# Kernel optimization log

Hardware: AMD Instinct MI355X
Metric: run time of the kernel (lower is better)

## Reference

```python
import jax, jax.numpy as jnp
import numpy as np

D_MODEL = 1024
N_HEAD = 16
POWER = 4
EPS = 1e-6
MASK_FILL = -1000.0


def setup_inputs() -> dict:
    key = jax.random.key(0)
    ks = jax.random.split(key, 10)
    B, T, C = 2, 2048, D_MODEL
    sc = 1.0 / np.sqrt(C)
    inp = {
        "x": jax.random.normal(ks[0], (B, T, C), jnp.float32),
        "Wq": jax.random.normal(ks[1], (C, C), jnp.float32) * sc,
        "bq": jnp.zeros((C,), jnp.float32),
        "Wk": jax.random.normal(ks[2], (C, C), jnp.float32) * sc,
        "bk": jnp.zeros((C,), jnp.float32),
        "Wv": jax.random.normal(ks[3], (C, C), jnp.float32) * sc,
        "bv": jnp.zeros((C,), jnp.float32),
        "Wo": jax.random.normal(ks[4], (C, C), jnp.float32) * sc,
        "bo": jnp.zeros((C,), jnp.float32),
        "score_gain": jnp.asarray(4.0, jnp.float32),
        # True above the diagonal -> masked (causal)
        "causal_mask": jnp.triu(jnp.ones((T, T), jnp.bool_), k=1),
    }
    return inp


def rational_softmax(x):
    s = x / (jnp.abs(x) + 1.0)          # squash to (-1, 1)
    p = ((s + 1.0) * 0.5) ** POWER      # (0,1) then sharpen
    return p / (jnp.sum(p, axis=-1, keepdims=True) + EPS)


def reference(x, Wq, bq, Wk, bk, Wv, bv, Wo, bo, score_gain, causal_mask):
    B, T, C = x.shape
    H, D = N_HEAD, C // N_HEAD
    q = (x @ Wq + bq).reshape(B, T, H, D)
    k = (x @ Wk + bk).reshape(B, T, H, D)
    v = (x @ Wv + bv).reshape(B, T, H, D)
    # scores: (B, H, T, T)
    scores = jnp.einsum('bqhd,bkhd->bhqk', q, k)
    scores = scores - jnp.mean(scores, axis=-1, keepdims=True)
    mad = jnp.mean(jnp.abs(scores), axis=-1, keepdims=True) + 1e-6
    scores = scores / mad * score_gain
    scores = jnp.where(causal_mask, MASK_FILL, scores)
    attn = rational_softmax(scores)
    out = jnp.einsum('bhqk,bkhd->bqhd', attn, v).reshape(B, T, C)
    return out @ Wo + bo
```

## Files before the change

### kernel.cpp

```cpp
#include <hip/hip_runtime.h>
#include <hip/hip_bf16.h>
#include <cstdint>

#define BDIM 2
#define TSEQ 2048
#define CDIM 1024
#define NH 16
#define HD 64
#define NTOK (BDIM*TSEQ)
#define MASK_FILL_V (-1000.0f)
#define EPS_V (1e-6f)

typedef short bf16x8 __attribute__((ext_vector_type(8)));
typedef float f32x4  __attribute__((ext_vector_type(4)));

__device__ __forceinline__ float bf2f(unsigned short u) {
    union { unsigned int i; float f; } x; x.i = ((unsigned int)u) << 16; return x.f;
}
__device__ __forceinline__ unsigned short f2bf(float v) {
    __hip_bfloat16 h = __float2bfloat16(v);
    union { __hip_bfloat16 h; unsigned short u; } c; c.h = h; return c.u;
}
__device__ __forceinline__ float unpk_lo(unsigned int u) {
    union { unsigned int i; float f; } x; x.i = u << 16; return x.f;
}
__device__ __forceinline__ float unpk_hi(unsigned int u) {
    union { unsigned int i; float f; } x; x.i = u & 0xFFFF0000u; return x.f;
}
__device__ __forceinline__ unsigned int pk2(float lo, float hi) {
    unsigned int r;
    asm("v_cvt_pk_bf16_f32 %0, %1, %2" : "=v"(r) : "v"(lo), "v"(hi));
    return r;
}

__device__ __forceinline__ bool dt_is_bf16(const void* gain_p) {
    return ((*(const unsigned int*)gain_p) & 0xFFFFu) == 0x4080u;
}
__device__ __forceinline__ float ld1(const void* p, size_t i, bool bf) {
    return bf ? bf2f(((const unsigned short*)p)[i]) : ((const float*)p)[i];
}

__device__ __forceinline__ void gl2lds16(const unsigned short* g, unsigned short* l) {
    __builtin_amdgcn_global_load_lds(
        (const __attribute__((address_space(1))) unsigned int*)g,
        (__attribute__((address_space(3))) unsigned int*)l, 16, 0, 0);
}

__global__ __launch_bounds__(256) void pack_x_kernel(
    const void* __restrict__ X, const void* __restrict__ gain_p,
    unsigned short* __restrict__ Xb)
{
    const bool bf = dt_is_bf16(gain_p);
    size_t i = ((size_t)blockIdx.x * 256 + threadIdx.x) * 8;
    if (bf) {
        *(bf16x8*)&Xb[i] = *(const bf16x8*)((const unsigned short*)X + i);
    } else {
        const float* xf = (const float*)X;
        float4 a = *(const float4*)&xf[i];
        float4 b = *(const float4*)&xf[i + 4];
        bf16x8 o;
        o[0]=(short)f2bf(a.x); o[1]=(short)f2bf(a.y); o[2]=(short)f2bf(a.z); o[3]=(short)f2bf(a.w);
        o[4]=(short)f2bf(b.x); o[5]=(short)f2bf(b.y); o[6]=(short)f2bf(b.z); o[7]=(short)f2bf(b.w);
        *(bf16x8*)&Xb[i] = o;
    }
}

__global__ __launch_bounds__(256) void pack_wt_kernel(
    const void* __restrict__ Wq, const void* __restrict__ Wk,
    const void* __restrict__ Wv, const void* __restrict__ Wo,
    const void* __restrict__ gain_p, unsigned short* __restrict__ Wt)
{
    __shared__ __align__(16) unsigned short tile[64][72];
    const bool bf = dt_is_bf16(gain_p);
    const int which = blockIdx.z;
    const void* W = (which == 0) ? Wq : (which == 1) ? Wk : (which == 2) ? Wv : Wo;
    const int k0 = blockIdx.y * 64, n0 = blockIdx.x * 64;
    const int t = threadIdx.x;
    const int r = t >> 2, cb = (t & 3) * 16;
    if (bf) {
        const unsigned short* wsd = (const unsigned short*)W;
        *(bf16x8*)&tile[r][cb]     = *(const bf16x8*)&wsd[(size_t)(k0 + r) * CDIM + n0 + cb];
        *(bf16x8*)&tile[r][cb + 8] = *(const bf16x8*)&wsd[(size_t)(k0 + r) * CDIM + n0 + cb + 8];
    } else {
        const float* wf = (const float*)W;
        const float* src = &wf[(size_t)(k0 + r) * CDIM + n0 + cb];
        float4 f0 = *(const float4*)&src[0];
        float4 f1 = *(const float4*)&src[4];
        float4 f2 = *(const float4*)&src[8];
        float4 f3 = *(const float4*)&src[12];
        bf16x8 o0, o1;
        o0[0]=(short)f2bf(f0.x); o0[1]=(short)f2bf(f0.y); o0[2]=(short)f2bf(f0.z); o0[3]=(short)f2bf(f0.w);
        o0[4]=(short)f2bf(f1.x); o0[5]=(short)f2bf(f1.y); o0[6]=(short)f2bf(f1.z); o0[7]=(short)f2bf(f1.w);
        o1[0]=(short)f2bf(f2.x); o1[1]=(short)f2bf(f2.y); o1[2]=(short)f2bf(f2.z); o1[3]=(short)f2bf(f2.w);
        o1[4]=(short)f2bf(f3.x); o1[5]=(short)f2bf(f3.y); o1[6]=(short)f2bf(f3.z); o1[7]=(short)f2bf(f3.w);
        *(bf16x8*)&tile[r][cb]     = o0;
        *(bf16x8*)&tile[r][cb + 8] = o1;
    }
    __syncthreads();
    const int dr = t >> 2, tb = (t & 3) * 16;
    __align__(16) unsigned short tmp[16];
#pragma unroll
    for (int j = 0; j < 16; ++j) tmp[j] = tile[tb + j][dr];
    unsigned short* dst = Wt + ((size_t)(which * CDIM + n0 + dr)) * CDIM + k0 + tb;
    *(bf16x8*)&dst[0] = *(bf16x8*)&tmp[0];
    *(bf16x8*)&dst[8] = *(bf16x8*)&tmp[8];
}

__global__ __launch_bounds__(256) void gemm_mfma_kernel(
    const unsigned short* __restrict__ A,
    const unsigned short* __restrict__ Bt,
    const void* __restrict__ b0p, const void* __restrict__ b1p,
    const void* __restrict__ b2p,
    const void* __restrict__ gain_p,
    unsigned short* __restrict__ qkv,
    void* __restrict__ outp, int mode)
{
    __shared__ __align__(16) unsigned short As[128 * 32];
    __shared__ __align__(16) unsigned short Bs[128 * 32];

    const bool bf = dt_is_bf16(gain_p);
    const int t = threadIdx.x;
    const int w = t >> 6, lane = t & 63, quad = lane >> 4, l16 = lane & 15;
    const int wm = w >> 1, wn = w & 1;
    const int n0 = blockIdx.x * 128, m0 = blockIdx.y * 128;

    const unsigned short* Ag = A  + (size_t)m0 * CDIM;
    const unsigned short* Bg = Bt + (size_t)n0 * CDIM;

    f32x4 acc[4][4];
#pragma unroll
    for (int mt = 0; mt < 4; ++mt)
#pragma unroll
        for (int nt = 0; nt < 4; ++nt)
            acc[mt][nt] = (f32x4){0.f, 0.f, 0.f, 0.f};

    for (int kt = 0; kt < CDIM / 32; ++kt) {
        const int k0 = kt * 32;
#pragma unroll
        for (int i = 0; i < 2; ++i) {
            const int chunk = (i * 4 + w) * 64 + lane;
            const int row = chunk >> 2, kp = (chunk & 3) * 8;
            gl2lds16(Ag + (size_t)row * CDIM + k0 + kp, &As[(i * 4 + w) * 512]);
            gl2lds16(Bg + (size_t)row * CDIM + k0 + kp, &Bs[(i * 4 + w) * 512]);
        }
        __syncthreads();
        bf16x8 af[4], bfr[4];
#pragma unroll
        for (int mt = 0; mt < 4; ++mt)
            af[mt] = *(const bf16x8*)&As[(wm * 64 + mt * 16 + l16) * 32 + quad * 8];
#pragma unroll
        for (int nt = 0; nt < 4; ++nt)
            bfr[nt] = *(const bf16x8*)&Bs[(wn * 64 + nt * 16 + l16) * 32 + quad * 8];
#pragma unroll
        for (int mt = 0; mt < 4; ++mt)
#pragma unroll
            for (int nt = 0; nt < 4; ++nt)
                acc[mt][nt] = __builtin_amdgcn_mfma_f32_16x16x32_bf16(af[mt], bfr[nt], acc[mt][nt], 0, 0, 0);
        __syncthreads();
    }

    if (mode == 0) {
        const int which = n0 >> 10;
        if (which < 2) {
            const void* biasP = (which == 0) ? b0p : b1p;
            unsigned short* out = qkv + (size_t)which * NTOK * CDIM;
#pragma unroll
            for (int nt = 0; nt < 4; ++nt) {
                const int np = (n0 & 1023) + wn * 64 + nt * 16 + l16;
                const int h = np >> 6, d = np & 63;
                const float bias = ld1(biasP, np, bf);
#pragma unroll
                for (int mt = 0; mt < 4; ++mt)
#pragma unroll
                    for (int r = 0; r < 4; ++r) {
                        const int m = m0 + wm * 64 + mt * 16 + quad * 4 + r;
                        const int bb = m >> 11, tt = m & (TSEQ - 1);
                        out[(((size_t)(bb * NH + h)) * TSEQ + tt) * HD + d] =
                            f2bf(acc[mt][nt][r] + bias);
                    }
            }
        } else {
            unsigned short* vt = (unsigned short*)outp;
#pragma unroll
            for (int nt = 0; nt < 4; ++nt) {
                const int np = (n0 & 1023) + wn * 64 + nt * 16 + l16;
                const int h = np >> 6, d = np & 63;
                const float bias = ld1(b2p, np, bf);
#pragma unroll
                for (int mt = 0; mt < 4; ++mt) {
                    const int m = m0 + wm * 64 + mt * 16 + quad * 4;
                    const int bb = m >> 11, tt0 = m & (TSEQ - 1);
                    unsigned int lo = ((unsigned int)f2bf(acc[mt][nt][1] + bias) << 16)
                                    |  (unsigned int)f2bf(acc[mt][nt][0] + bias);
                    unsigned int hi = ((unsigned int)f2bf(acc[mt][nt][3] + bias) << 16)
                                    |  (unsigned int)f2bf(acc[mt][nt][2] + bias);
                    uint2 pk; pk.x = lo; pk.y = hi;
                    *(uint2*)&vt[((size_t)(bb * NH + h) * HD + d) * TSEQ + tt0] = pk;
                }
            }
        }
    } else {
#pragma unroll
        for (int nt = 0; nt < 4; ++nt) {
            const int np = n0 + wn * 64 + nt * 16 + l16;
            const float bias = ld1(b0p, np, bf);
#pragma unroll
            for (int mt = 0; mt < 4; ++mt)
#pragma unroll
                for (int r = 0; r < 4; ++r) {
                    const int m = m0 + wm * 64 + mt * 16 + quad * 4 + r;
                    const float v = acc[mt][nt][r] + bias;
                    if (bf) ((__hip_bfloat16*)outp)[(size_t)m * CDIM + np] = __float2bfloat16(v);
                    else    ((float*)outp)[(size_t)m * CDIM + np] = v;
                }
        }
    }
}

__global__ __launch_bounds__(256) void ksum_kernel(
    const unsigned short* __restrict__ Kb, float* __restrict__ Ksum)
{
    __shared__ float red[32][64];
    const int bh = blockIdx.x;
    const int t = threadIdx.x;
    const int d8 = (t & 7) * 8, g = t >> 3;
    const unsigned short* kp = Kb + (size_t)bh * TSEQ * HD;
    float s[8] = {};
    for (int tt = g; tt < TSEQ; tt += 32) {
        bf16x8 v = *(const bf16x8*)&kp[(size_t)tt * HD + d8];
#pragma unroll
        for (int j = 0; j < 8; ++j) s[j] += bf2f((unsigned short)v[j]);
    }
#pragma unroll
    for (int j = 0; j < 8; ++j) red[g][d8 + j] = s[j];
    __syncthreads();
    if (t < 64) {
        float tot = 0.f;
#pragma unroll
        for (int gg = 0; gg < 32; ++gg) tot += red[gg][t];
        Ksum[(size_t)bh * HD + t] = tot;
    }
}

#define QROWS 16
#define NQT (TSEQ / QROWS)

__global__ __launch_bounds__(512, 2) void attn_mfma_kernel(
    const unsigned short* __restrict__ Qb,
    const unsigned short* __restrict__ Kb,
    const unsigned short* __restrict__ Vt,
    const float* __restrict__ Ksum,
    const void* __restrict__ gain_p,
    unsigned short* __restrict__ AOb)
{
    __shared__ float smad[2][8][16];
    __shared__ float spsum[2][8][16];
    __shared__ float pvp[8][16 * 68];

    const bool bf = dt_is_bf16(gain_p);
    const float gain = ld1(gain_p, 0, bf);

    const int t    = threadIdx.x;
    const int w    = t >> 6;
    const int lane = t & 63;
    const int quad = lane >> 4;
    const int l16  = lane & 15;
    const int b4   = quad & 1, b5 = quad >> 1;

    const int id = blockIdx.x;
    const int bh = id & 31;
    const int p  = id >> 5;
    const int q0a = p * QROWS;
    const int q0b = (NQT - 1 - p) * QROWS;
    const int b  = bh >> 4, h = bh & 15;
    const size_t base = (size_t)bh * TSEQ * HD;

    bf16x8 qfA[2], qfB[2];
    qfA[0] = *(const bf16x8*)&Qb[base + (size_t)(q0a + l16) * HD + quad * 8];
    qfA[1] = *(const bf16x8*)&Qb[base + (size_t)(q0a + l16) * HD + 32 + quad * 8];
    qfB[0] = *(const bf16x8*)&Qb[base + (size_t)(q0b + l16) * HD + quad * 8];
    qfB[1] = *(const bf16x8*)&Qb[base + (size_t)(q0b + l16) * HD + 32 + quad * 8];

    const float* Ks = Ksum + (size_t)bh * HD;
    float4 kA0 = *(const float4*)&Ks[quad * 8];
    float4 kA1 = *(const float4*)&Ks[quad * 8 + 4];
    float4 kB0 = *(const float4*)&Ks[32 + quad * 8];
    float4 kB1 = *(const float4*)&Ks[32 + quad * 8 + 4];
    auto qdot = [&](const bf16x8 (&qf)[2]) -> float {
        float m;
        m  = bf2f((unsigned short)qf[0][0]) * kA0.x;
        m  = fmaf(bf2f((unsigned short)qf[0][1]), kA0.y, m);
        m  = fmaf(bf2f((unsigned short)qf[0][2]), kA0.z, m);
        m  = fmaf(bf2f((unsigned short)qf[0][3]), kA0.w, m);
        m  = fmaf(bf2f((unsigned short)qf[0][4]), kA1.x, m);
        m  = fmaf(bf2f((unsigned short)qf[0][5]), kA1.y, m);
        m  = fmaf(bf2f((unsigned short)qf[0][6]), kA1.z, m);
        m  = fmaf(bf2f((unsigned short)qf[0][7]), kA1.w, m);
        m  = fmaf(bf2f((unsigned short)qf[1][0]), kB0.x, m);
        m  = fmaf(bf2f((unsigned short)qf[1][1]), kB0.y, m);
        m  = fmaf(bf2f((unsigned short)qf[1][2]), kB0.z, m);
        m  = fmaf(bf2f((unsigned short)qf[1][3]), kB0.w, m);
        m  = fmaf(bf2f((unsigned short)qf[1][4]), kB1.x, m);
        m  = fmaf(bf2f((unsigned short)qf[1][5]), kB1.y, m);
        m  = fmaf(bf2f((unsigned short)qf[1][6]), kB1.z, m);
        m  = fmaf(bf2f((unsigned short)qf[1][7]), kB1.w, m);
        m += __shfl_xor(m, 16);
        m += __shfl_xor(m, 32);
        return m * (1.0f / TSEQ);
    };
    const float meanA = qdot(qfA);
    const float meanB = qdot(qfB);

    const unsigned short* kp = Kb + base + (size_t)(w * 16 + l16) * HD + quad * 8;
    bf16x8 kbuf[4][2];
#pragma unroll
    for (int i = 0; i < 4; ++i) {
        kbuf[i][0] = *(const bf16x8*)&kp[(size_t)i * 8192];
        kbuf[i][1] = *(const bf16x8*)&kp[(size_t)i * 8192 + 32];
    }

    unsigned int pkwA[8][2], pkwB[16][2];
    float madpA0 = 0.f, madpA1 = 0.f, madpB0 = 0.f, madpB1 = 0.f;
#pragma unroll
    for (int i = 0; i < 16; ++i) {
        bf16x8 c0 = kbuf[i & 3][0], c1 = kbuf[i & 3][1];
        if (i + 4 < 16) {
            kbuf[i & 3][0] = *(const bf16x8*)&kp[(size_t)(i + 4) * 8192];
            kbuf[i & 3][1] = *(const bf16x8*)&kp[(size_t)(i + 4) * 8192 + 32];
        }
        f32x4 z = (f32x4){0.f, 0.f, 0.f, 0.f};
        f32x4 sA0 = __builtin_amdgcn_mfma_f32_16x16x32_bf16(c0, qfA[0], z, 0, 0, 0);
        f32x4 sA1 = __builtin_amdgcn_mfma_f32_16x16x32_bf16(c1, qfA[1], z, 0, 0, 0);
        f32x4 sB0 = __builtin_amdgcn_mfma_f32_16x16x32_bf16(c0, qfB[0], z, 0, 0, 0);
        f32x4 sB1 = __builtin_amdgcn_mfma_f32_16x16x32_bf16(c1, qfB[1], z, 0, 0, 0);
        float a0 = (sA0[0] + sA1[0]) - meanA, a1 = (sA0[1] + sA1[1]) - meanA;
        float a2 = (sA0[2] + sA1[2]) - meanA, a3 = (sA0[3] + sA1[3]) - meanA;
        madpA0 += fabsf(a0) + fabsf(a1);
        madpA1 += fabsf(a2) + fabsf(a3);
        if (i < 8) {
            pkwA[i][0] = pk2(a0, a1);
            pkwA[i][1] = pk2(a2, a3);
        }
        float e0 = (sB0[0] + sB1[0]) - meanB, e1 = (sB0[1] + sB1[1]) - meanB;
        float e2 = (sB0[2] + sB1[2]) - meanB, e3 = (sB0[3] + sB1[3]) - meanB;
        madpB0 += fabsf(e0) + fabsf(e1);
        madpB1 += fabsf(e2) + fabsf(e3);
        pkwB[i][0] = pk2(e0, e1);
        pkwB[i][1] = pk2(e2, e3);
    }
    float madpA = madpA0 + madpA1;
    float madpB = madpB0 + madpB1;
    madpA += __shfl_xor(madpA, 16);
    madpA += __shfl_xor(madpA, 32);
    madpB += __shfl_xor(madpB, 16);
    madpB += __shfl_xor(madpB, 32);
    if (lane < 16) { smad[0][w][lane] = madpA; smad[1][w][lane] = madpB; }
    __syncthreads();

    float msA = 0.f, msB = 0.f;
#pragma unroll
    for (int ww = 0; ww < 8; ++ww) { msA += smad[0][ww][l16]; msB += smad[1][ww][l16]; }
    const float scaleA = gain / (msA * (1.0f / TSEQ) + 1e-6f);
    const float scaleB = gain / (msB * (1.0f / TSEQ) + 1e-6f);

    const int NTmaxA = p;
    const int NTmaxB = NQT - 1 - p;
    const int difA = NTmaxA - w;
    const int i_maxA = (difA >= 0) ? (difA >> 3) : -1;
    const int jmaxA  = (i_maxA >= 0) ? (i_maxA >> 1) : -1;
    const int difB = NTmaxB - w;
    const int i_maxB = (difB >= 0) ? (difB >> 3) : -1;
    const int jmaxB  = (i_maxB >= 0) ? (i_maxB >> 1) : -1;

    const bool kgt0 = (quad * 4 + 0) > l16;
    const bool kgt1 = (quad * 4 + 1) > l16;
    const bool kgt2 = (quad * 4 + 2) > l16;
    const bool kgt3 = (quad * 4 + 3) > l16;

    auto rsoft = [](float vv) -> float {
        float rc = __builtin_amdgcn_rcpf(fabsf(vv) + 1.0f);
        float ss = vv * rc;
        float u  = fmaf(ss, 0.5f, 0.5f);
        float u2 = u * u;
        return u2 * u2;
    };
    auto xform = [&](unsigned int plo, unsigned int phi, bool mask, float scale,
                     float& psum, unsigned int& P0, unsigned int& P1) {
        float v0 = unpk_lo(plo) * scale, v1 = unpk_hi(plo) * scale;
        float v2 = unpk_lo(phi) * scale, v3 = unpk_hi(phi) * scale;
        if (mask) {
            if (kgt0) v0 = MASK_FILL_V;
            if (kgt1) v1 = MASK_FILL_V;
            if (kgt2) v2 = MASK_FILL_V;
            if (kgt3) v3 = MASK_FILL_V;
        }
        float p0 = rsoft(v0), p1 = rsoft(v1), p2 = rsoft(v2), p3 = rsoft(v3);
        psum += (p0 + p1) + (p2 + p3);
        P0 = pk2(p0, p1);
        P1 = pk2(p2, p3);
    };
    auto exch = [&](const unsigned int (&pk0)[2], const unsigned int (&pk1)[2],
                    bool use1, bool mask0, bool mask1, float scale,
                    float& psum, unsigned int (&fru)[4]) {
        unsigned int A0, A1, B0, B1;
        xform(pk0[0], pk0[1], mask0, scale, psum, A0, A1);
        if (use1) xform(pk1[0], pk1[1], mask1, scale, psum, B0, B1);
        else { B0 = 0u; B1 = 0u; }
        unsigned int K0 = b5 ? B0 : A0, K1 = b5 ? B1 : A1;
        unsigned int T0 = b5 ? A0 : B0, T1 = b5 ? A1 : B1;
        unsigned int R0 = (unsigned int)__shfl_xor((int)T0, 32);
        unsigned int R1 = (unsigned int)__shfl_xor((int)T1, 32);
        unsigned int S0 = (b5 ^ b4) ? K0 : R0, S1 = (b5 ^ b4) ? K1 : R1;
        unsigned int U0 = (unsigned int)__shfl_xor((int)S0, 16);
        unsigned int U1 = (unsigned int)__shfl_xor((int)S1, 16);
        fru[0] = b4 ? U0 : (b5 ? R0 : K0);
        fru[1] = b4 ? U1 : (b5 ? R1 : K1);
        fru[2] = b4 ? (b5 ? K0 : R0) : U0;
        fru[3] = b4 ? (b5 ? K1 : R1) : U1;
    };

    const unsigned short* vp = Vt + ((size_t)bh * HD + l16) * TSEQ
                               + w * 16 + b5 * 128 + b4 * 8;

    float psumA = 0.f, psumB = 0.f;
    f32x4 aA0 = (f32x4){0.f,0.f,0.f,0.f}, aA1 = (f32x4){0.f,0.f,0.f,0.f};
    f32x4 aA2 = (f32x4){0.f,0.f,0.f,0.f}, aA3 = (f32x4){0.f,0.f,0.f,0.f};
    f32x4 aB0 = (f32x4){0.f,0.f,0.f,0.f}, aB1 = (f32x4){0.f,0.f,0.f,0.f};
    f32x4 aB2 = (f32x4){0.f,0.f,0.f,0.f}, aB3 = (f32x4){0.f,0.f,0.f,0.f};
#pragma unroll
    for (int j = 0; j < 8; ++j) {
        if (j <= jmaxB) {
            bf16x8 vb0 = *(const bf16x8*)&vp[j * 256 + 0 * 32768];
            bf16x8 vb1 = *(const bf16x8*)&vp[j * 256 + 1 * 32768];
            bf16x8 vb2 = *(const bf16x8*)&vp[j * 256 + 2 * 32768];
            bf16x8 vb3 = *(const bf16x8*)&vp[j * 256 + 3 * 32768];
            unsigned int fruB[4];
            exch(pkwB[2 * j], pkwB[2 * j + 1], (2 * j + 1) <= i_maxB,
                 (w + 16 * j) == NTmaxB, (w + 16 * j + 8) == NTmaxB,
                 scaleB, psumB, fruB);
            union { unsigned int u[4]; bf16x8 v; } FB;
            FB.u[0] = fruB[0]; FB.u[1] = fruB[1]; FB.u[2] = fruB[2]; FB.u[3] = fruB[3];
            aB0 = __builtin_amdgcn_mfma_f32_16x16x32_bf16(FB.v, vb0, aB0, 0, 0, 0);
            aB1 = __builtin_amdgcn_mfma_f32_16x16x32_bf16(FB.v, vb1, aB1, 0, 0, 0);
            aB2 = __builtin_amdgcn_mfma_f32_16x16x32_bf16(FB.v, vb2, aB2, 0, 0, 0);
            aB3 = __builtin_amdgcn_mfma_f32_16x16x32_bf16(FB.v, vb3, aB3, 0, 0, 0);
            if (j < 4) {
                if (j <= jmaxA) {
                    unsigned int fruA[4];
                    exch(pkwA[2 * j], pkwA[2 * j + 1], (2 * j + 1) <= i_maxA,
                         (w + 16 * j) == NTmaxA, (w + 16 * j + 8) == NTmaxA,
                         scaleA, psumA, fruA);
                    union { unsigned int u[4]; bf16x8 v; } FA;
                    FA.u[0] = fruA[0]; FA.u[1] = fruA[1]; FA.u[2] = fruA[2]; FA.u[3] = fruA[3];
                    aA0 = __builtin_amdgcn_mfma_f32_16x16x32_bf16(FA.v, vb0, aA0, 0, 0, 0);
                    aA1 = __builtin_amdgcn_mfma_f32_16x16x32_bf16(FA.v, vb1, aA1, 0, 0, 0);
                    aA2 = __builtin_amdgcn_mfma_f32_16x16x32_bf16(FA.v, vb2, aA2, 0, 0, 0);
                    aA3 = __builtin_amdgcn_mfma_f32_16x16x32_bf16(FA.v, vb3, aA3, 0, 0, 0);
                }
            }
        }
    }

    psumA += __shfl_xor(psumA, 16);
    psumA += __shfl_xor(psumA, 32);
    psumB += __shfl_xor(psumB, 16);
    psumB += __shfl_xor(psumB, 32);
    if (lane < 16) { spsum[0][w][lane] = psumA; spsum[1][w][lane] = psumB; }

#pragma unroll
    for (int r = 0; r < 4; ++r) {
        const int qi = quad * 4 + r;
        pvp[w][qi * 68 +      l16] = aA0[r];
        pvp[w][qi * 68 + 16 + l16] = aA1[r];
        pvp[w][qi * 68 + 32 + l16] = aA2[r];
        pvp[w][qi * 68 + 48 + l16] = aA3[r];
    }
    __syncthreads();
    {
        const int q  = t >> 5;
        const int d2 = (t & 31) * 2;
        float s0 = 0.f, s1 = 0.f;
#pragma unroll
        for (int ww = 0; ww < 8; ++ww) {
            const float* pp = &pvp[ww][q * 68 + d2];
            s0 += pp[0];
            s1 += pp[1];
        }
        float ps = 0.f;
#pragma unroll
        for (int ww = 0; ww < 8; ++ww) ps += spsum[0][ww][q];
        const float inv = 1.0f / (ps + EPS_V);
        unsigned int o = ((unsigned int)f2bf(s1 * inv) << 16) | (unsigned int)f2bf(s0 * inv);
        *(unsigned int*)&AOb[((size_t)(b * TSEQ + q0a + q)) * CDIM + h * HD + d2] = o;
    }
    __syncthreads();

#pragma unroll
    for (int r = 0; r < 4; ++r) {
        const int qi = quad * 4 + r;
        pvp[w][qi * 68 +      l16] = aB0[r];
        pvp[w][qi * 68 + 16 + l16] = aB1[r];
        pvp[w][qi * 68 + 32 + l16] = aB2[r];
        pvp[w][qi * 68 + 48 + l16] = aB3[r];
    }
    __syncthreads();
    {
        const int q  = t >> 5;
        const int d2 = (t & 31) * 2;
        float s0 = 0.f, s1 = 0.f;
#pragma unroll
        for (int ww = 0; ww < 8; ++ww) {
            const float* pp = &pvp[ww][q * 68 + d2];
            s0 += pp[0];
            s1 += pp[1];
        }
        float ps = 0.f;
#pragma unroll
        for (int ww = 0; ww < 8; ++ww) ps += spsum[1][ww][q];
        const float inv = 1.0f / (ps + EPS_V);
        unsigned int o = ((unsigned int)f2bf(s1 * inv) << 16) | (unsigned int)f2bf(s0 * inv);
        *(unsigned int*)&AOb[((size_t)(b * TSEQ + q0b + q)) * CDIM + h * HD + d2] = o;
    }
}

extern "C" void kernel_launch(void* const* d_in, const int* in_sizes, int n_in,
                              void* d_out, int out_size, void* d_ws, size_t ws_size,
                              hipStream_t stream)
{
    (void)in_sizes; (void)n_in; (void)out_size; (void)ws_size;
    const void* X    = d_in[0];
    const void* Wq   = d_in[1];
    const void* bq   = d_in[2];
    const void* Wk   = d_in[3];
    const void* bk   = d_in[4];
    const void* Wv   = d_in[5];
    const void* bv   = d_in[6];
    const void* Wo   = d_in[7];
    const void* bo   = d_in[8];
    const void* gain = d_in[9];

    char* ws = (char*)d_ws;
    unsigned short* Xb  = (unsigned short*)ws;
    unsigned short* Wt  = (unsigned short*)(ws + (8ull  << 20));
    unsigned short* QKV = (unsigned short*)(ws + (16ull << 20));
    unsigned short* Vt  = (unsigned short*)(ws + (40ull << 20));
    unsigned short* AOb = (unsigned short*)(ws + (48ull << 20));
    float*          Ks  = (float*)(ws + (56ull << 20));
    unsigned short* Qb  = QKV;
    unsigned short* Kb  = QKV + (size_t)NTOK * CDIM;

    pack_x_kernel<<<NTOK * CDIM / (256 * 8), 256, 0, stream>>>(X, gain, Xb);
    pack_wt_kernel<<<dim3(16, 16, 4), 256, 0, stream>>>(Wq, Wk, Wv, Wo, gain, Wt);

    dim3 g1(3 * CDIM / 128, NTOK / 128);
    gemm_mfma_kernel<<<g1, 256, 0, stream>>>(Xb, Wt, bq, bk, bv, gain, QKV, Vt, 0);

    ksum_kernel<<<BDIM * NH, 256, 0, stream>>>(Kb, Ks);

    attn_mfma_kernel<<<(NQT / 2) * BDIM * NH, 512, 0, stream>>>(
        Qb, Kb, Vt, Ks, gain, AOb);

    dim3 g3(CDIM / 128, NTOK / 128);
    gemm_mfma_kernel<<<g3, 256, 0, stream>>>(AOb, Wt + 3ull * CDIM * CDIM, bo, bo, bo, gain,
                                             nullptr, d_out, 1);
}
```

Baseline: 309.7 us.

## Swizzle GEMM block order, fold mean into MFMA init, prefetch V, set MFMA priority

The GEMM remaps block indices so consecutive workgroups are spread across eight groups, aiming at better L2/XCD locality. In attention, the mean subtraction is folded into the MFMA accumulator init, which saves some VALU subtracts. The first V tile is now prefetched before the MAD reduction barrier so its load latency overlaps the sync. MFMA groups are also wrapped in s_setprio so the scheduler favours matrix issue. The swizzle assumes the grid size divides by eight.

```diff
diff --git a/kernel.cpp b/kernel.cpp
--- a/kernel.cpp
+++ b/kernel.cpp
@@ -122,7 +122,12 @@
     const int t = threadIdx.x;
     const int w = t >> 6, lane = t & 63, quad = lane >> 4, l16 = lane & 15;
     const int wm = w >> 1, wn = w & 1;
-    const int n0 = blockIdx.x * 128, m0 = blockIdx.y * 128;
+
+    const int gx = gridDim.x, gy = gridDim.y;
+    const int lin = blockIdx.y * gx + blockIdx.x;
+    const int chunk = (gx * gy) >> 3;
+    const int nid = (lin & 7) * chunk + (lin >> 3);
+    const int n0 = (nid / gy) * 128, m0 = (nid % gy) * 128;
 
     const unsigned short* Ag = A  + (size_t)m0 * CDIM;
     const unsigned short* Bg = Bt + (size_t)n0 * CDIM;
@@ -138,8 +143,8 @@
         const int k0 = kt * 32;
 #pragma unroll
         for (int i = 0; i < 2; ++i) {
-            const int chunk = (i * 4 + w) * 64 + lane;
-            const int row = chunk >> 2, kp = (chunk & 3) * 8;
+            const int chunkid = (i * 4 + w) * 64 + lane;
+            const int row = chunkid >> 2, kp = (chunkid & 3) * 8;
             gl2lds16(Ag + (size_t)row * CDIM + k0 + kp, &As[(i * 4 + w) * 512]);
             gl2lds16(Bg + (size_t)row * CDIM + k0 + kp, &Bs[(i * 4 + w) * 512]);
         }
@@ -310,6 +315,8 @@
     };
     const float meanA = qdot(qfA);
     const float meanB = qdot(qfB);
+    const f32x4 cinitA = (f32x4){-meanA, -meanA, -meanA, -meanA};
+    const f32x4 cinitB = (f32x4){-meanB, -meanB, -meanB, -meanB};
 
     const unsigned short* kp = Kb + base + (size_t)(w * 16 + l16) * HD + quad * 8;
     bf16x8 kbuf[4][2];
@@ -329,20 +336,20 @@
             kbuf[i & 3][1] = *(const bf16x8*)&kp[(size_t)(i + 4) * 8192 + 32];
         }
         f32x4 z = (f32x4){0.f, 0.f, 0.f, 0.f};
-        f32x4 sA0 = __builtin_amdgcn_mfma_f32_16x16x32_bf16(c0, qfA[0], z, 0, 0, 0);
+        f32x4 sA0 = __builtin_amdgcn_mfma_f32_16x16x32_bf16(c0, qfA[0], cinitA, 0, 0, 0);
         f32x4 sA1 = __builtin_amdgcn_mfma_f32_16x16x32_bf16(c1, qfA[1], z, 0, 0, 0);
-        f32x4 sB0 = __builtin_amdgcn_mfma_f32_16x16x32_bf16(c0, qfB[0], z, 0, 0, 0);
+        f32x4 sB0 = __builtin_amdgcn_mfma_f32_16x16x32_bf16(c0, qfB[0], cinitB, 0, 0, 0);
         f32x4 sB1 = __builtin_amdgcn_mfma_f32_16x16x32_bf16(c1, qfB[1], z, 0, 0, 0);
-        float a0 = (sA0[0] + sA1[0]) - meanA, a1 = (sA0[1] + sA1[1]) - meanA;
-        float a2 = (sA0[2] + sA1[2]) - meanA, a3 = (sA0[3] + sA1[3]) - meanA;
+        float a0 = sA0[0] + sA1[0], a1 = sA0[1] + sA1[1];
+        float a2 = sA0[2] + sA1[2], a3 = sA0[3] + sA1[3];
         madpA0 += fabsf(a0) + fabsf(a1);
         madpA1 += fabsf(a2) + fabsf(a3);
         if (i < 8) {
             pkwA[i][0] = pk2(a0, a1);
             pkwA[i][1] = pk2(a2, a3);
         }
-        float e0 = (sB0[0] + sB1[0]) - meanB, e1 = (sB0[1] + sB1[1]) - meanB;
-        float e2 = (sB0[2] + sB1[2]) - meanB, e3 = (sB0[3] + sB1[3]) - meanB;
+        float e0 = sB0[0] + sB1[0], e1 = sB0[1] + sB1[1];
+        float e2 = sB0[2] + sB1[2], e3 = sB0[3] + sB1[3];
         madpB0 += fabsf(e0) + fabsf(e1);
         madpB1 += fabsf(e2) + fabsf(e3);
         pkwB[i][0] = pk2(e0, e1);
@@ -355,6 +362,14 @@
     madpB += __shfl_xor(madpB, 16);
     madpB += __shfl_xor(madpB, 32);
     if (lane < 16) { smad[0][w][lane] = madpA; smad[1][w][lane] = madpB; }
+
+    const unsigned short* vp = Vt + ((size_t)bh * HD + l16) * TSEQ
+                               + w * 16 + b5 * 128 + b4 * 8;
+    bf16x8 vpre0 = *(const bf16x8*)&vp[0 * 32768];
+    bf16x8 vpre1 = *(const bf16x8*)&vp[1 * 32768];
+    bf16x8 vpre2 = *(const bf16x8*)&vp[2 * 32768];
+    bf16x8 vpre3 = *(const bf16x8*)&vp[3 * 32768];
+
     __syncthreads();
 
     float msA = 0.f, msB = 0.f;
@@ -419,9 +434,6 @@
         fru[3] = b4 ? (b5 ? K1 : R1) : U1;
     };
 
-    const unsigned short* vp = Vt + ((size_t)bh * HD + l16) * TSEQ
-                               + w * 16 + b5 * 128 + b4 * 8;
-
     float psumA = 0.f, psumB = 0.f;
     f32x4 aA0 = (f32x4){0.f,0.f,0.f,0.f}, aA1 = (f32x4){0.f,0.f,0.f,0.f};
     f32x4 aA2 = (f32x4){0.f,0.f,0.f,0.f}, aA3 = (f32x4){0.f,0.f,0.f,0.f};
@@ -430,20 +442,22 @@
 #pragma unroll
     for (int j = 0; j < 8; ++j) {
         if (j <= jmaxB) {
-            bf16x8 vb0 = *(const bf16x8*)&vp[j * 256 + 0 * 32768];
-            bf16x8 vb1 = *(const bf16x8*)&vp[j * 256 + 1 * 32768];
-            bf16x8 vb2 = *(const bf16x8*)&vp[j * 256 + 2 * 32768];
-            bf16x8 vb3 = *(const bf16x8*)&vp[j * 256 + 3 * 32768];
+            bf16x8 vb0 = (j == 0) ? vpre0 : *(const bf16x8*)&vp[j * 256 + 0 * 32768];
+            bf16x8 vb1 = (j == 0) ? vpre1 : *(const bf16x8*)&vp[j * 256 + 1 * 32768];
+            bf16x8 vb2 = (j == 0) ? vpre2 : *(const bf16x8*)&vp[j * 256 + 2 * 32768];
+            bf16x8 vb3 = (j == 0) ? vpre3 : *(const bf16x8*)&vp[j * 256 + 3 * 32768];
             unsigned int fruB[4];
             exch(pkwB[2 * j], pkwB[2 * j + 1], (2 * j + 1) <= i_maxB,
                  (w + 16 * j) == NTmaxB, (w + 16 * j + 8) == NTmaxB,
                  scaleB, psumB, fruB);
             union { unsigned int u[4]; bf16x8 v; } FB;
             FB.u[0] = fruB[0]; FB.u[1] = fruB[1]; FB.u[2] = fruB[2]; FB.u[3] = fruB[3];
+            __builtin_amdgcn_s_setprio(1);
             aB0 = __builtin_amdgcn_mfma_f32_16x16x32_bf16(FB.v, vb0, aB0, 0, 0, 0);
             aB1 = __builtin_amdgcn_mfma_f32_16x16x32_bf16(FB.v, vb1, aB1, 0, 0, 0);
             aB2 = __builtin_amdgcn_mfma_f32_16x16x32_bf16(FB.v, vb2, aB2, 0, 0, 0);
             aB3 = __builtin_amdgcn_mfma_f32_16x16x32_bf16(FB.v, vb3, aB3, 0, 0, 0);
+            __builtin_amdgcn_s_setprio(0);
             if (j < 4) {
                 if (j <= jmaxA) {
                     unsigned int fruA[4];
@@ -452,10 +466,12 @@
                          scaleA, psumA, fruA);
                     union { unsigned int u[4]; bf16x8 v; } FA;
                     FA.u[0] = fruA[0]; FA.u[1] = fruA[1]; FA.u[2] = fruA[2]; FA.u[3] = fruA[3];
+                    __builtin_amdgcn_s_setprio(1);
                     aA0 = __builtin_amdgcn_mfma_f32_16x16x32_bf16(FA.v, vb0, aA0, 0, 0, 0);
                     aA1 = __builtin_amdgcn_mfma_f32_16x16x32_bf16(FA.v, vb1, aA1, 0, 0, 0);
                     aA2 = __builtin_amdgcn_mfma_f32_16x16x32_bf16(FA.v, vb2, aA2, 0, 0, 0);
                     aA3 = __builtin_amdgcn_mfma_f32_16x16x32_bf16(FA.v, vb3, aA3, 0, 0, 0);
+                    __builtin_amdgcn_s_setprio(0);
                 }
             }
         }
```

Result: slower. 325.8 us (+5.2%).
